# Optimization experiments

Hardware: AMD Instinct MI355X
Metric: run time of the kernel (lower is better)

## Reference

```python
import jax, jax.numpy as jnp
import numpy as np

N_NODES = 131072
N_EDGES = 2097152
B = 256
NODES_PER_GRAPH = 512  # uniform graphs -> to_dense_batch == reshape
F_IN = 74
D = 128
L = 3
EPS = 1e-5


def setup_inputs() -> dict:
    key = jax.random.key(0)
    ks = jax.random.split(key, 12)
    x = jax.random.normal(ks[0], (N_NODES, F_IN), dtype=jnp.float32)
    edge_index = jax.random.randint(ks[1], (2, N_EDGES), 0, N_NODES, dtype=jnp.int32)
    batch = (jnp.arange(N_NODES, dtype=jnp.int32) // NODES_PER_GRAPH)
    s = 1.0 / np.sqrt(D)
    W_init = jax.random.uniform(ks[2], (F_IN, D), jnp.float32, -s, s)
    W_gcn = jax.random.uniform(ks[3], (L, D, D), jnp.float32, -s, s)
    b_gcn = jnp.zeros((L, D), jnp.float32)
    gamma = jnp.ones((L, D), jnp.float32)
    beta = jnp.zeros((L, D), jnp.float32)
    W_res = jax.random.uniform(ks[4], (L, D, D), jnp.float32, -s, s)
    b_res = jax.random.uniform(ks[5], (L, D), jnp.float32, -s, s)
    return {"x": x, "edge_index": edge_index, "batch": batch, "W_init": W_init,
            "W_gcn": W_gcn, "b_gcn": b_gcn, "gamma": gamma, "beta": beta,
            "W_res": W_res, "b_res": b_res}


def _gcn_conv(x, src, tgt, norm, W, b):
    # PyG GCNConv: h = x @ W ; out[tgt] += norm * h[src] ; + bias
    h = x @ W                                    # [N, D]
    msg = h[src] * norm[:, None]                 # [E+N, D] gather (memory-bound)
    out = jax.ops.segment_sum(msg, tgt, num_segments=N_NODES)
    return out + b


def _batchnorm(x, g, bta):
    mean = jnp.mean(x, axis=0)
    var = jnp.var(x, axis=0)  # biased, matches torch BN training forward
    return (x - mean) * jax.lax.rsqrt(var + EPS) * g + bta


def reference(x, edge_index, batch, W_init, W_gcn, b_gcn, gamma, beta, W_res, b_res):
    # add self loops once; symmetric deg^{-1/2} normalization (PyG default)
    loops = jnp.arange(N_NODES, dtype=edge_index.dtype)
    src = jnp.concatenate([edge_index[0], loops])
    tgt = jnp.concatenate([edge_index[1], loops])
    deg = jax.ops.segment_sum(jnp.ones_like(src, dtype=jnp.float32), tgt,
                              num_segments=N_NODES)
    dinv = jnp.where(deg > 0, jax.lax.rsqrt(jnp.maximum(deg, 1.0)), 0.0)
    norm = dinv[src] * dinv[tgt]

    h = x @ W_init                               # init_transform (no bias)
    for i in range(L):
        conv = _gcn_conv(h, src, tgt, norm, W_gcn[i], b_gcn[i])
        h_new = jax.nn.relu(_batchnorm(conv, gamma[i], beta[i]))
        h = h_new + (h @ W_res[i] + b_res[i])
    # to_dense_batch with uniform NODES_PER_GRAPH -> reshape, all mask=True
    return h.reshape(B, NODES_PER_GRAPH, D)
```

## Files before the change

### kernel.cpp

```cpp
#include <hip/hip_runtime.h>

#define NN 131072
#define NE 2097152
#define DD 128
#define LL 3

#define NB 256
#define BSH 9
#define TILE (NE / NB)

typedef __attribute__((ext_vector_type(8))) short short8;
typedef __attribute__((ext_vector_type(4))) float f32x4;

__device__ __forceinline__ ushort f2bf(float f) {
    uint u = __float_as_uint(f);
    return (ushort)((u + 0x7fffu + ((u >> 16) & 1u)) >> 16);
}
__device__ __forceinline__ float bflo(uint u) { return __uint_as_float(u << 16); }
__device__ __forceinline__ float bfhi(uint u) { return __uint_as_float(u & 0xffff0000u); }

__global__ __launch_bounds__(256) void k_prep(const float* __restrict__ x,
                                              const float* __restrict__ Wi,
                                              const float* __restrict__ Wg,
                                              const float* __restrict__ Wr,
                                              uint* __restrict__ xb,
                                              ushort* __restrict__ wt,
                                              float* __restrict__ bns) {
    const int t = threadIdx.x, blk = blockIdx.x;
    const size_t id = (size_t)blk * 256 + t;
    const int n = (int)(id >> 6);
    const int k0 = (int)(id & 63) * 2;
    float v0 = (k0 < 74) ? x[(size_t)n * 74 + k0] : 0.0f;
    float v1 = (k0 + 1 < 74) ? x[(size_t)n * 74 + k0 + 1] : 0.0f;
    xb[id] = (uint)f2bf(v0) | ((uint)f2bf(v1) << 16);
    if (blk < 448) {
        const int id2 = blk * 256 + t;
        const int m = id2 >> 14;
        const int c = (id2 >> 7) & 127;
        const int k = id2 & 127;
        float v;
        if (m == 0)      v = (k < 74) ? Wi[k * DD + c] : 0.0f;
        else if (m <= 3) v = Wg[(size_t)(m - 1) * DD * DD + k * DD + c];
        else             v = Wr[(size_t)(m - 4) * DD * DD + k * DD + c];
        wt[id2] = f2bf(v);
    }
    if (blk == 448) {
        bns[t] = 0.0f; bns[t + 256] = 0.0f; bns[t + 512] = 0.0f;
    }
}

__global__ __launch_bounds__(256) void kA_count(const int* __restrict__ tgt,
                                                int* __restrict__ blockHist) {
    __shared__ int hist[NB];
    const int t = threadIdx.x, blk = blockIdx.x;
    hist[t] = 0;
    __syncthreads();
    const int base = blk * TILE;
#pragma unroll 8
    for (int j = 0; j < TILE / 256; ++j)
        atomicAdd(&hist[tgt[base + j * 256 + t] >> BSH], 1);
    __syncthreads();
    blockHist[t * NB + blk] = hist[t];
}

__global__ __launch_bounds__(256) void kA_scan1(int* __restrict__ blockHist,
                                                int* __restrict__ rowSum) {
    __shared__ int sc[256];
    const int t = threadIdx.x, b = blockIdx.x;
    const int v = blockHist[b * NB + t];
    sc[t] = v;
    __syncthreads();
    for (int off = 1; off < 256; off <<= 1) {
        int a = sc[t];
        int u = (t >= off) ? sc[t - off] : 0;
        __syncthreads();
        sc[t] = a + u;
        __syncthreads();
    }
    blockHist[b * NB + t] = sc[t] - v;
    if (t == 255) rowSum[b] = sc[255];
}

__global__ __launch_bounds__(256) void kA_scan2(const int* __restrict__ rowSum,
                                                int* __restrict__ bstart) {
    __shared__ int sc[256];
    const int t = threadIdx.x;
    const int v = rowSum[t];
    sc[t] = v;
    __syncthreads();
    for (int off = 1; off < 256; off <<= 1) {
        int a = sc[t];
        int u = (t >= off) ? sc[t - off] : 0;
        __syncthreads();
        sc[t] = a + u;
        __syncthreads();
    }
    bstart[t] = sc[t] - v;
    if (t == 255) bstart[NB] = sc[255];
}

__global__ __launch_bounds__(256) void kA_scatter(const int* __restrict__ src,
                                                  const int* __restrict__ tgt,
                                                  const int* __restrict__ chunkBase,
                                                  const int* __restrict__ bstart,
                                                  uint* __restrict__ packed) {
    __shared__ int cur[NB];
    const int t = threadIdx.x, blk = blockIdx.x;
    cur[t] = bstart[t] + chunkBase[t * NB + blk];
    __syncthreads();
    const int base = blk * TILE;
#pragma unroll 4
    for (int j = 0; j < TILE / 256; ++j) {
        const int e = base + j * 256 + t;
        const int tg = tgt[e], s = src[e];
        const int b = tg >> BSH;
        const int pos = atomicAdd(&cur[b], 1);
        packed[pos] = (uint)s | ((uint)(tg & ((1 << BSH) - 1)) << 17);
    }
}

__global__ __launch_bounds__(256) void kB_sort(const uint* __restrict__ packed,
                                               const int* __restrict__ bstart,
                                               int* __restrict__ rowp,
                                               float* __restrict__ dinv,
                                               int* __restrict__ deg,
                                               int* __restrict__ ssrc) {
    __shared__ int cnt[1 << BSH];
    __shared__ int pscan[256];
    const int t = threadIdx.x, b = blockIdx.x;
    const int e0 = bstart[b], e1 = bstart[b + 1];
    cnt[t] = 0; cnt[t + 256] = 0;
    __syncthreads();
    for (int e = e0 + t; e < e1; e += 256)
        atomicAdd(&cnt[packed[e] >> 17], 1);
    __syncthreads();
    const int c0 = cnt[2 * t], c1 = cnt[2 * t + 1];
    pscan[t] = c0 + c1;
    __syncthreads();
    for (int off = 1; off < 256; off <<= 1) {
        int v = pscan[t];
        int u = (t >= off) ? pscan[t - off] : 0;
        __syncthreads();
        pscan[t] = v + u;
        __syncthreads();
    }
    const int ex0 = pscan[t] - c0 - c1;
    const int ex1 = ex0 + c0;
    const int n0 = (b << BSH) + 2 * t;
    rowp[n0] = e0 + ex0;
    rowp[n0 + 1] = e0 + ex1;
    dinv[n0] = rsqrtf((float)(c0 + 1));
    dinv[n0 + 1] = rsqrtf((float)(c1 + 1));
    deg[n0] = c0 + 1;
    deg[n0 + 1] = c1 + 1;
    if (b == NB - 1 && t == 255) rowp[NN] = e1;
    __syncthreads();
    cnt[2 * t] = ex0;
    cnt[2 * t + 1] = ex1;
    __syncthreads();
    for (int e = e0 + t; e < e1; e += 256) {
        const uint p = packed[e];
        const int tl = p >> 17;
        const int pos = atomicAdd(&cnt[tl], 1);
        ssrc[e0 + pos] = (int)(p & 0x1FFFFu);
    }
}

__global__ __launch_bounds__(256) void k_pack(int* __restrict__ ssrc,
                                              const int* __restrict__ deg) {
    const int e = blockIdx.x * 256 + threadIdx.x;
    const int s = ssrc[e];
    ssrc[e] = s | (deg[s] << 17);
}

template <int MODE>
__global__ __launch_bounds__(256) void k_mgemm(const ushort* __restrict__ A,
                                               const ushort* __restrict__ Bt,
                                               ushort* outb,
                                               float* __restrict__ outf,
                                               const ushort* __restrict__ convb,
                                               const float* __restrict__ gamma,
                                               const float* __restrict__ beta,
                                               const float* __restrict__ bres,
                                               float* __restrict__ bnsums) {
    __shared__ ushort Bs[16384];
    __shared__ float sred[256];
    const int t = threadIdx.x;
    const int w = t >> 6, l = t & 63;
    const int lc = l & 15, lr = l >> 4;
    const size_t row0 = (size_t)blockIdx.x * 128;

    for (int ch = w * 8; ch < w * 8 + 8; ++ch) {
        const int row = ch * 4 + lr;
        const int kb = (lc * 16) ^ ((row & 7) << 4);
        const ushort* srcB = Bt + (size_t)row * DD + (kb >> 1);
        __builtin_amdgcn_global_load_lds(
            (const __attribute__((address_space(1))) void*)srcB,
            (__attribute__((address_space(3))) void*)(Bs + ch * 512), 16, 0, 0);
    }
    if (MODE == 1) sred[t] = 0.0f;
    if (MODE >= 2 && t < DD) {
        const float invN = 1.0f / (float)NN;
        const float mean = bnsums[t] * invN;
        const float var = bnsums[DD + t] * invN - mean * mean;
        const float sc = gamma[t] * rsqrtf(var + 1e-5f);
        sred[t] = sc;
        sred[DD + t] = beta[t] - mean * sc;
    }
    __syncthreads();

    short8 a[2][4];
#pragma unroll
    for (int m = 0; m < 2; ++m) {
        const ushort* Arow = A + (row0 + w * 32 + m * 16 + lc) * DD + lr * 8;
#pragma unroll
        for (int kk = 0; kk < 4; ++kk)
            a[m][kk] = *(const short8*)(Arow + kk * 32);
    }

    f32x4 acc[2][8] = {};
    const char* Bb = (const char*)Bs;
#pragma unroll
    for (int kk = 0; kk < 4; ++kk) {
        const int kb = kk * 64 + lr * 16;
#pragma unroll
        for (int n = 0; n < 8; ++n) {
            const int c = n * 16 + lc;
            short8 b = *(const short8*)(Bb + c * 256 + (kb ^ ((c & 7) << 4)));
            acc[0][n] = __builtin_amdgcn_mfma_f32_16x16x32_bf16(a[0][kk], b, acc[0][n], 0, 0, 0);
            acc[1][n] = __builtin_amdgcn_mfma_f32_16x16x32_bf16(a[1][kk], b, acc[1][n], 0, 0, 0);
        }
    }

    if (MODE == 0) {
#pragma unroll
        for (int m = 0; m < 2; ++m)
#pragma unroll
            for (int n = 0; n < 8; ++n) {
                const int c = n * 16 + lc;
#pragma unroll
                for (int j = 0; j < 4; ++j) {
                    const size_t r = row0 + w * 32 + m * 16 + lr * 4 + j;
                    outb[r * DD + c] = f2bf(acc[m][n][j]);
                }
            }
    } else if (MODE == 1) {
#pragma unroll
        for (int n = 0; n < 8; ++n) {
            const int c = n * 16 + lc;
            float ps = 0.0f, ps2 = 0.0f;
#pragma unroll
            for (int m = 0; m < 2; ++m)
#pragma unroll
                for (int j = 0; j < 4; ++j) {
                    const size_t r = row0 + w * 32 + m * 16 + lr * 4 + j;
                    const float v = acc[m][n][j];
                    outb[r * DD + c] = f2bf(v);
                    ps += v; ps2 += v * v;
                }
            atomicAdd(&sred[c], ps);
            atomicAdd(&sred[DD + c], ps2);
        }
        __syncthreads();
        atomicAdd(&bnsums[t], sred[t]);
    } else {
        float scv[8], shv[8], bbv[8];
#pragma unroll
        for (int n = 0; n < 8; ++n) {
            const int c = n * 16 + lc;
            scv[n] = sred[c]; shv[n] = sred[DD + c]; bbv[n] = bres[c];
        }
#pragma unroll
        for (int m = 0; m < 2; ++m)
#pragma unroll
            for (int n = 0; n < 8; ++n) {
                const int c = n * 16 + lc;
#pragma unroll
                for (int j = 0; j < 4; ++j) {
                    const size_t r = row0 + w * 32 + m * 16 + lr * 4 + j;
                    const float cv = __uint_as_float((uint)convb[r * DD + c] << 16);
                    const float v = fmaxf(cv * scv[n] + shv[n], 0.0f) + acc[m][n][j] + bbv[n];
                    if (MODE == 2) outb[r * DD + c] = f2bf(v);
                    if (MODE == 3) outf[r * DD + c] = v;
                }
            }
    }
}

__global__ __launch_bounds__(256) void k_aggregate(const int* __restrict__ rowp,
                                                   const float* __restrict__ dinv,
                                                   const int* __restrict__ ssrc,
                                                   const uint* __restrict__ hb,
                                                   uint* __restrict__ aggb) {
    __shared__ float2 eb[4][64];
    const int wv = threadIdx.x >> 6;
    const int n = blockIdx.x * 4 + wv;
    const int l = threadIdx.x & 63;
    const float dn = dinv[n];
    const uint u0 = hb[((uint)n << 6) + l];
    const float dn2 = dn * dn;
    float ax = dn2 * bflo(u0), ay = dn2 * bfhi(u0);
    const int e0 = rowp[n], e1 = rowp[n + 1];
    for (int base = e0; base < e1; base += 64) {
        const int cnt = min(64, e1 - base);
        float nm = 0.0f; uint sb = 0;
        if (l < cnt) {
            const uint p = (uint)ssrc[base + l];
            sb = (p & 0x1FFFFu) << 6;
            nm = dn * rsqrtf((float)(p >> 17));
        }
        eb[wv][l] = make_float2(nm, __uint_as_float(sb));
        int i = 0;
        for (; i + 16 <= cnt; i += 16) {
            uint vv[16]; float nmv[16];
#pragma unroll
            for (int j = 0; j < 16; ++j) {
                const float2 e = eb[wv][i + j];
                nmv[j] = e.x;
                vv[j] = hb[__float_as_uint(e.y) + l];
            }
#pragma unroll
            for (int j = 0; j < 16; ++j) {
                ax += nmv[j] * bflo(vv[j]);
                ay += nmv[j] * bfhi(vv[j]);
            }
        }
        for (; i < cnt; i += 8) {
            uint vv[8]; float nmv[8];
#pragma unroll
            for (int j = 0; j < 8; ++j) {
                const float2 e = eb[wv][i + j];
                nmv[j] = e.x;
                vv[j] = hb[__float_as_uint(e.y) + l];
            }
#pragma unroll
            for (int j = 0; j < 8; ++j) {
                ax += nmv[j] * bflo(vv[j]);
                ay += nmv[j] * bfhi(vv[j]);
            }
        }
    }
    aggb[((uint)n << 6) + l] = (uint)f2bf(ax) | ((uint)f2bf(ay) << 16);
}

extern "C" void kernel_launch(void* const* d_in, const int* in_sizes, int n_in,
                              void* d_out, int out_size, void* d_ws, size_t ws_size,
                              hipStream_t stream) {
    const float* x      = (const float*)d_in[0];
    const int*   ei     = (const int*)d_in[1];
    const float* W_init = (const float*)d_in[3];
    const float* W_gcn  = (const float*)d_in[4];
    const float* gamma  = (const float*)d_in[6];
    const float* beta   = (const float*)d_in[7];
    const float* W_res  = (const float*)d_in[8];
    const float* b_res  = (const float*)d_in[9];

    float* h = (float*)d_out;
    char* p = (char*)d_ws;
    ushort* aggb = (ushort*)p;           p += (size_t)NN * DD * 2;
    ushort* hb   = (ushort*)p;           p += (size_t)NN * DD * 2;
    ushort* convb = (ushort*)p;          p += (size_t)NN * DD * 2;
    uint*   xb   = (uint*)convb;
    float*  dinv = (float*)p;            p += (size_t)NN * 4;
    int*    deg  = (int*)p;              p += (size_t)NN * 4;
    float*  bns  = (float*)p;            p += 768 * 4;
    ushort* wt   = (ushort*)p;           p += 7 * 16384 * 2;
    int* blockHist = (int*)p;            p += (size_t)NB * NB * 4;
    int* rowSum  = (int*)p;              p += NB * 4;
    int* bstart  = (int*)p;              p += (NB + 1) * 4 + 4;
    uint* packed = (uint*)p;             p += (size_t)NE * 4;
    int* rowp    = (int*)p;              p += ((size_t)NN + 1) * 4 + 4;
    int* ssrc    = (int*)p;

    const int* srcp = ei;
    const int* tgtp = ei + NE;

    k_prep<<<NN * 64 / 256, 256, 0, stream>>>(x, W_init, W_gcn, W_res, xb, wt, bns);
    kA_count<<<NB, 256, 0, stream>>>(tgtp, blockHist);
    kA_scan1<<<NB, 256, 0, stream>>>(blockHist, rowSum);
    kA_scan2<<<1, 256, 0, stream>>>(rowSum, bstart);
    kA_scatter<<<NB, 256, 0, stream>>>(srcp, tgtp, blockHist, bstart, packed);
    kB_sort<<<NB, 256, 0, stream>>>(packed, bstart, rowp, dinv, deg, ssrc);
    k_pack<<<NE / 256, 256, 0, stream>>>(ssrc, deg);

    k_mgemm<0><<<NN / 128, 256, 0, stream>>>((const ushort*)xb, wt, hb,
                                             nullptr, nullptr, nullptr, nullptr,
                                             nullptr, nullptr);

    for (int i = 0; i < LL; ++i) {
        k_aggregate<<<NN / 4, 256, 0, stream>>>(rowp, dinv, ssrc,
                                                (const uint*)hb, (uint*)aggb);
        k_mgemm<1><<<NN / 128, 256, 0, stream>>>(aggb, wt + (size_t)(1 + i) * 16384,
                                                 convb, nullptr, nullptr, nullptr,
                                                 nullptr, nullptr, bns + i * 256);
        if (i < LL - 1)
            k_mgemm<2><<<NN / 128, 256, 0, stream>>>(hb, wt + (size_t)(4 + i) * 16384,
                                                     hb, nullptr, convb,
                                                     gamma + i * DD, beta + i * DD,
                                                     b_res + i * DD, bns + i * 256);
        else
            k_mgemm<3><<<NN / 128, 256, 0, stream>>>(hb, wt + (size_t)(4 + i) * 16384,
                                                     nullptr, h, convb,
                                                     gamma + i * DD, beta + i * DD,
                                                     b_res + i * DD, bns + i * 256);
    }
}
```

Measured before the change: 558.2 us.

## Fuse bucket scan into scatter, stage GEMM A tile via LDS, nontemporal edge loads

The single-block scan2 kernel is folded into kA_scatter: every block redoes the 256-entry scan and block 0 writes bstart, which removes one launch. The MFMA GEMM now copies its A tile into swizzled LDS with global_load_lds alongside B, instead of loading A fragments from global memory into registers. This adds 32KB of LDS per block, which may lower occupancy. In k_aggregate the edge-index loads use nontemporal hints to reduce cache pollution.

```diff
diff --git a/kernel.cpp b/kernel.cpp
--- a/kernel.cpp
+++ b/kernel.cpp
@@ -81,10 +81,15 @@
     if (t == 255) rowSum[b] = sc[255];
 }
 
-__global__ __launch_bounds__(256) void kA_scan2(const int* __restrict__ rowSum,
-                                                int* __restrict__ bstart) {
+__global__ __launch_bounds__(256) void kA_scatter(const int* __restrict__ src,
+                                                  const int* __restrict__ tgt,
+                                                  const int* __restrict__ chunkBase,
+                                                  const int* __restrict__ rowSum,
+                                                  int* __restrict__ bstart,
+                                                  uint* __restrict__ packed) {
+    __shared__ int cur[NB];
     __shared__ int sc[256];
-    const int t = threadIdx.x;
+    const int t = threadIdx.x, blk = blockIdx.x;
     const int v = rowSum[t];
     sc[t] = v;
     __syncthreads();
@@ -95,18 +100,12 @@
         sc[t] = a + u;
         __syncthreads();
     }
-    bstart[t] = sc[t] - v;
-    if (t == 255) bstart[NB] = sc[255];
-}
-
-__global__ __launch_bounds__(256) void kA_scatter(const int* __restrict__ src,
-                                                  const int* __restrict__ tgt,
-                                                  const int* __restrict__ chunkBase,
-                                                  const int* __restrict__ bstart,
-                                                  uint* __restrict__ packed) {
-    __shared__ int cur[NB];
-    const int t = threadIdx.x, blk = blockIdx.x;
-    cur[t] = bstart[t] + chunkBase[t * NB + blk];
+    const int bst = sc[t] - v;
+    cur[t] = bst + chunkBase[t * NB + blk];
+    if (blk == 0) {
+        bstart[t] = bst;
+        if (t == 255) bstart[NB] = sc[255];
+    }
     __syncthreads();
     const int base = blk * TILE;
 #pragma unroll 4
@@ -174,7 +173,7 @@
 }
 
 template <int MODE>
-__global__ __launch_bounds__(256) void k_mgemm(const ushort* __restrict__ A,
+__global__ __launch_bounds__(256) void k_mgemm(const ushort* A,
                                                const ushort* __restrict__ Bt,
                                                ushort* outb,
                                                float* __restrict__ outf,
@@ -183,6 +182,7 @@
                                                const float* __restrict__ beta,
                                                const float* __restrict__ bres,
                                                float* __restrict__ bnsums) {
+    __shared__ ushort As[16384];
     __shared__ ushort Bs[16384];
     __shared__ float sred[256];
     const int t = threadIdx.x;
@@ -193,7 +193,11 @@
     for (int ch = w * 8; ch < w * 8 + 8; ++ch) {
         const int row = ch * 4 + lr;
         const int kb = (lc * 16) ^ ((row & 7) << 4);
+        const ushort* srcA = A + (row0 + row) * DD + (kb >> 1);
         const ushort* srcB = Bt + (size_t)row * DD + (kb >> 1);
+        __builtin_amdgcn_global_load_lds(
+            (const __attribute__((address_space(1))) void*)srcA,
+            (__attribute__((address_space(3))) void*)(As + ch * 512), 16, 0, 0);
         __builtin_amdgcn_global_load_lds(
             (const __attribute__((address_space(1))) void*)srcB,
             (__attribute__((address_space(3))) void*)(Bs + ch * 512), 16, 0, 0);
@@ -209,26 +213,24 @@
     }
     __syncthreads();
 
-    short8 a[2][4];
-#pragma unroll
-    for (int m = 0; m < 2; ++m) {
-        const ushort* Arow = A + (row0 + w * 32 + m * 16 + lc) * DD + lr * 8;
-#pragma unroll
-        for (int kk = 0; kk < 4; ++kk)
-            a[m][kk] = *(const short8*)(Arow + kk * 32);
-    }
-
     f32x4 acc[2][8] = {};
+    const char* Ab = (const char*)As;
     const char* Bb = (const char*)Bs;
 #pragma unroll
     for (int kk = 0; kk < 4; ++kk) {
         const int kb = kk * 64 + lr * 16;
+        short8 a[2];
+#pragma unroll
+        for (int m = 0; m < 2; ++m) {
+            const int r = w * 32 + m * 16 + lc;
+            a[m] = *(const short8*)(Ab + r * 256 + (kb ^ ((r & 7) << 4)));
+        }
 #pragma unroll
         for (int n = 0; n < 8; ++n) {
             const int c = n * 16 + lc;
             short8 b = *(const short8*)(Bb + c * 256 + (kb ^ ((c & 7) << 4)));
-            acc[0][n] = __builtin_amdgcn_mfma_f32_16x16x32_bf16(a[0][kk], b, acc[0][n], 0, 0, 0);
-            acc[1][n] = __builtin_amdgcn_mfma_f32_16x16x32_bf16(a[1][kk], b, acc[1][n], 0, 0, 0);
+            acc[0][n] = __builtin_amdgcn_mfma_f32_16x16x32_bf16(a[0], b, acc[0][n], 0, 0, 0);
+            acc[1][n] = __builtin_amdgcn_mfma_f32_16x16x32_bf16(a[1], b, acc[1][n], 0, 0, 0);
         }
     }
 
@@ -305,7 +307,7 @@
         const int cnt = min(64, e1 - base);
         float nm = 0.0f; uint sb = 0;
         if (l < cnt) {
-            const uint p = (uint)ssrc[base + l];
+            const uint p = (uint)__builtin_nontemporal_load(ssrc + base + l);
             sb = (p & 0x1FFFFu) << 6;
             nm = dn * rsqrtf((float)(p >> 17));
         }
@@ -378,8 +380,7 @@
     k_prep<<<NN * 64 / 256, 256, 0, stream>>>(x, W_init, W_gcn, W_res, xb, wt, bns);
     kA_count<<<NB, 256, 0, stream>>>(tgtp, blockHist);
     kA_scan1<<<NB, 256, 0, stream>>>(blockHist, rowSum);
-    kA_scan2<<<1, 256, 0, stream>>>(rowSum, bstart);
-    kA_scatter<<<NB, 256, 0, stream>>>(srcp, tgtp, blockHist, bstart, packed);
+    kA_scatter<<<NB, 256, 0, stream>>>(srcp, tgtp, blockHist, rowSum, bstart, packed);
     kB_sort<<<NB, 256, 0, stream>>>(packed, bstart, rowp, dinv, deg, ssrc);
     k_pack<<<NE / 256, 256, 0, stream>>>(ssrc, deg);
 
```

After: 529.8 us. -5.1%, faster.
